# Kernel optimization log

Measured on AMD Instinct MI355X. Metric: run time of the kernel, lower is better.

## Reference

```python
import jax, jax.numpy as jnp
import numpy as np

B, S, D = 16, 2048, 128

def setup_inputs() -> dict:
    key = jax.random.key(0)
    k1, k2, k3 = jax.random.split(key, 3)
    return {
        "query": jax.random.normal(k1, (B, S, D), dtype=jnp.float32),
        "key": jax.random.normal(k2, (B, S, D), dtype=jnp.float32),
        "value": jax.random.normal(k3, (B, S, D), dtype=jnp.float32),
    }

def reference(query, key, value):
    dq = query.shape[-1]
    dk = key.shape[-1]
    # custom scale: sqrt(Dq) + sqrt(Dk - Dq); with Dq == Dk this is sqrt(Dq)
    inv_scale = np.sqrt(dq) + np.sqrt(dk - dq)
    qk = jnp.einsum("bqd,bkd->bqk", query, key) / jnp.float32(inv_scale)
    attn = jax.nn.softmax(qk, axis=-1)  # dropout_p=0 -> identity
    return jnp.einsum("bqk,bkd->bqd", attn, value)
```

## Files before the change

### kernel.cpp

```cpp
#include <hip/hip_runtime.h>
#include <stdint.h>

#define Bn 16
#define Sn 2048
#define Dn 128
#define QBLK 64
#define KVBLK 64
#define NTHR 256
#define NT (Sn / KVBLK)

typedef __attribute__((ext_vector_type(4))) float f32x4;
typedef __attribute__((ext_vector_type(16))) float f32x16;
typedef __attribute__((ext_vector_type(8))) short bf16x8;
typedef __attribute__((ext_vector_type(2))) unsigned int u32x2;

#define SMEM_BYTES 33792

__device__ __forceinline__ uint32_t f2bf_u(float f) {
  return (__float_as_uint(f) + 0x8000u) >> 16;
}
__device__ __forceinline__ uint32_t pk2(float a, float b) {
  return f2bf_u(a) | (f2bf_u(b) << 16);
}

__global__ __launch_bounds__(256) void tr_k(const float* __restrict__ K,
                                            unsigned short* __restrict__ Kf) {
  __shared__ unsigned short lds[64 * 136];
  const int tid = threadIdx.x;
  const float* src = K + (size_t)blockIdx.x * (64 * Dn);
#pragma unroll
  for (int it = 0; it < 8; ++it) {
    const int gr = it * 256 + tid;
    const int k = gr >> 5, g4 = gr & 31;
    const float4 v = ((const float4*)src)[gr];
    unsigned short* p = &lds[k * 136 + g4 * 4];
    p[0] = (unsigned short)f2bf_u(v.x);
    p[1] = (unsigned short)f2bf_u(v.y);
    p[2] = (unsigned short)f2bf_u(v.z);
    p[3] = (unsigned short)f2bf_u(v.w);
  }
  __syncthreads();
  char* dst = (char*)Kf + (size_t)blockIdx.x * 16384;
#pragma unroll
  for (int it = 0; it < 4; ++it) {
    const int g = it * 256 + tid;
    const int lane = g & 63, dk = (g >> 6) & 7, h = g >> 9;
    const int row = 32 * h + (lane & 31);
    const int d0 = dk * 16 + 8 * (lane >> 5);
    const unsigned short* p = &lds[row * 136 + d0];
    uint4 o;
    o.x = (uint32_t)p[0] | ((uint32_t)p[1] << 16);
    o.y = (uint32_t)p[2] | ((uint32_t)p[3] << 16);
    o.z = (uint32_t)p[4] | ((uint32_t)p[5] << 16);
    o.w = (uint32_t)p[6] | ((uint32_t)p[7] << 16);
    *(uint4*)(dst + g * 16) = o;
  }
}

__global__ __launch_bounds__(256) void tr_v(const float* __restrict__ V,
                                            unsigned short* __restrict__ Vf) {
  __shared__ unsigned short lds[64 * 130];
  const int tid = threadIdx.x;
  const float* src = V + (size_t)blockIdx.x * (64 * Dn);
#pragma unroll
  for (int it = 0; it < 8; ++it) {
    const int gr = it * 256 + tid;
    const int k = gr >> 5, g4 = gr & 31;
    const float4 v = ((const float4*)src)[gr];
    unsigned short* p = &lds[k * 130 + g4 * 4];
    p[0] = (unsigned short)f2bf_u(v.x);
    p[1] = (unsigned short)f2bf_u(v.y);
    p[2] = (unsigned short)f2bf_u(v.z);
    p[3] = (unsigned short)f2bf_u(v.w);
  }
  __syncthreads();
  char* dst = (char*)Vf + (size_t)blockIdx.x * 16384;
#pragma unroll
  for (int it = 0; it < 4; ++it) {
    const int g = it * 256 + tid;
    const int lane = g & 63, f3 = (g >> 6) & 7, h = g >> 9;
    const int d = (f3 >> 1) * 32 + (lane & 31);
    const int k0 = 32 * h + (f3 & 1) * 16 + 8 * (lane >> 5);
    uint4 o;
    o.x = (uint32_t)lds[(k0 + 0) * 130 + d] | ((uint32_t)lds[(k0 + 1) * 130 + d] << 16);
    o.y = (uint32_t)lds[(k0 + 2) * 130 + d] | ((uint32_t)lds[(k0 + 3) * 130 + d] << 16);
    o.z = (uint32_t)lds[(k0 + 4) * 130 + d] | ((uint32_t)lds[(k0 + 5) * 130 + d] << 16);
    o.w = (uint32_t)lds[(k0 + 6) * 130 + d] | ((uint32_t)lds[(k0 + 7) * 130 + d] << 16);
    *(uint4*)(dst + g * 16) = o;
  }
}

__global__ __launch_bounds__(NTHR, 2) void attn_fwd(
    const float* __restrict__ Q, const unsigned short* __restrict__ Kf,
    const unsigned short* __restrict__ Vf, float* __restrict__ O) {
  __shared__ uint4 smem_[SMEM_BYTES / 16];
  char* smem = (char*)smem_;

  const int tid = threadIdx.x;
  const int lane = tid & 63;
  const int w = tid >> 6;
  const int qw = w & 1;
  const int h = w >> 1;
  const int hi = lane >> 5;
  const int ql = lane & 31;

  const int i = blockIdx.x;
  const int j = i >> 3;
  const int b = (i & 7) + 8 * (j & 1);
  const int q0 = (j >> 1) * QBLK;
  const int qg = q0 + qw * 32 + ql;

  const float qscale = 0.08838834764831845f * 1.44269504088896340736f;
  bf16x8 qf[8];
  {
    const float* qrow = Q + (size_t)(b * Sn + qg) * Dn;
#pragma unroll
    for (int dk = 0; dk < 8; ++dk) {
      const int d0 = dk * 16 + hi * 8;
      const float4 a = *(const float4*)(qrow + d0);
      const float4 d = *(const float4*)(qrow + d0 + 4);
      bf16x8 q8;
      q8[0] = (short)f2bf_u(a.x * qscale); q8[1] = (short)f2bf_u(a.y * qscale);
      q8[2] = (short)f2bf_u(a.z * qscale); q8[3] = (short)f2bf_u(a.w * qscale);
      q8[4] = (short)f2bf_u(d.x * qscale); q8[5] = (short)f2bf_u(d.y * qscale);
      q8[6] = (short)f2bf_u(d.z * qscale); q8[7] = (short)f2bf_u(d.w * qscale);
      qf[dk] = q8;
    }
  }

  f32x16 o[4];
#pragma unroll
  for (int dt = 0; dt < 4; ++dt) {
#pragma unroll
    for (int jj = 0; jj < 16; ++jj) o[dt][jj] = 0.f;
  }
  float m_r = -1.0e30f, l_r = 0.f;

  const char* Kg = (const char*)(Kf + (size_t)b * Sn * Dn);
  const char* Vg = (const char*)(Vf + (size_t)b * Sn * Dn);

#pragma unroll 2
  for (int t = 0; t < NT; ++t) {
    bf16x8 kfr[8], vfr[8];
    {
      const char* kt = Kg + (size_t)t * 16384 + h * 8192 + lane * 16;
      const char* vt = Vg + (size_t)t * 16384 + h * 8192 + lane * 16;
#pragma unroll
      for (int f = 0; f < 8; ++f) kfr[f] = *(const bf16x8*)(kt + f * 1024);
#pragma unroll
      for (int f = 0; f < 8; ++f) vfr[f] = *(const bf16x8*)(vt + f * 1024);
    }

    f32x16 s;
#pragma unroll
    for (int jj = 0; jj < 16; ++jj) s[jj] = 0.f;
    __builtin_amdgcn_s_setprio(1);
#pragma unroll
    for (int dk = 0; dk < 8; ++dk)
      s = __builtin_amdgcn_mfma_f32_32x32x16_bf16(kfr[dk], qf[dk], s, 0, 0, 0);
    __builtin_amdgcn_s_setprio(0);

    float x0 = fmaxf(fmaxf(s[0], s[1]), fmaxf(s[2], s[3]));
    float x1 = fmaxf(fmaxf(s[4], s[5]), fmaxf(s[6], s[7]));
    float x2 = fmaxf(fmaxf(s[8], s[9]), fmaxf(s[10], s[11]));
    float x3 = fmaxf(fmaxf(s[12], s[13]), fmaxf(s[14], s[15]));
    float pm = fmaxf(fmaxf(x0, x1), fmaxf(x2, x3));
    pm = fmaxf(pm, __shfl_xor(pm, 32, 64));

    if (!__all(pm <= m_r + 8.0f)) {
      const float mnew = fmaxf(m_r, pm);
      const float alpha = __builtin_amdgcn_exp2f(m_r - mnew);
      l_r *= alpha;
#pragma unroll
      for (int dt = 0; dt < 4; ++dt) o[dt] *= alpha;
      m_r = mnew;
    }

#pragma unroll
    for (int jj = 0; jj < 16; ++jj) s[jj] = __builtin_amdgcn_exp2f(s[jj] - m_r);
    {
      float r0 = 0.f, r1 = 0.f, r2 = 0.f, r3 = 0.f;
#pragma unroll
      for (int jj = 0; jj < 4; ++jj) {
        r0 += s[jj]; r1 += s[4 + jj]; r2 += s[8 + jj]; r3 += s[12 + jj];
      }
      float rsum = (r0 + r1) + (r2 + r3);
      l_r += rsum + __shfl_xor(rsum, 32, 64);
    }

    uint32_t own[4][2];
#pragma unroll
    for (int mm = 0; mm < 4; ++mm) {
      own[mm][0] = pk2(s[4 * mm + 0], s[4 * mm + 1]);
      own[mm][1] = pk2(s[4 * mm + 2], s[4 * mm + 3]);
    }
    uint32_t rcv[2][2];
#pragma unroll
    for (int jj = 0; jj < 2; ++jj)
#pragma unroll
      for (int e = 0; e < 2; ++e) {
        uint32_t sel = hi ? own[2 * jj][e] : own[2 * jj + 1][e];
        rcv[jj][e] = (uint32_t)__shfl_xor((int)sel, 32, 64);
      }
    bf16x8 pb[2];
#pragma unroll
    for (int ks = 0; ks < 2; ++ks) {
      union { uint32_t u[4]; bf16x8 v; } tt;
      tt.u[0] = hi ? rcv[ks][0] : own[2 * ks][0];
      tt.u[1] = hi ? rcv[ks][1] : own[2 * ks][1];
      tt.u[2] = hi ? own[2 * ks + 1][0] : rcv[ks][0];
      tt.u[3] = hi ? own[2 * ks + 1][1] : rcv[ks][1];
      pb[ks] = tt.v;
    }

    __builtin_amdgcn_s_setprio(1);
#pragma unroll
    for (int dt = 0; dt < 4; ++dt) {
#pragma unroll
      for (int ks = 0; ks < 2; ++ks) {
        o[dt] = __builtin_amdgcn_mfma_f32_32x32x16_bf16(vfr[dt * 2 + ks], pb[ks],
                                                        o[dt], 0, 0, 0);
      }
    }
    __builtin_amdgcn_s_setprio(0);
  }

  __syncthreads();
  char* xch = smem + qw * 16896;
  if (h) {
#pragma unroll
    for (int dt = 0; dt < 4; ++dt) {
#pragma unroll
      for (int q2 = 0; q2 < 4; ++q2) {
        float4 v;
        v.x = o[dt][4 * q2 + 0]; v.y = o[dt][4 * q2 + 1];
        v.z = o[dt][4 * q2 + 2]; v.w = o[dt][4 * q2 + 3];
        *(float4*)(xch + (dt * 4 + q2) * 1024 + lane * 16) = v;
      }
    }
    *(float2*)(xch + 16384 + lane * 8) = make_float2(m_r, l_r);
  }
  __syncthreads();
  if (!h) {
    const float2 ml1v = *(const float2*)(xch + 16384 + lane * 8);
    const float M = fmaxf(m_r, ml1v.x);
    const float w0 = __builtin_amdgcn_exp2f(m_r - M);
    const float w1 = __builtin_amdgcn_exp2f(ml1v.x - M);
    const float inv = 1.0f / (l_r * w0 + ml1v.y * w1);
    const float s0 = w0 * inv, s1 = w1 * inv;
    float* orow = O + (size_t)(b * Sn + qg) * Dn;
#pragma unroll
    for (int dt = 0; dt < 4; ++dt) {
#pragma unroll
      for (int q2 = 0; q2 < 4; ++q2) {
        const float4 o1v =
            *(const float4*)(xch + (dt * 4 + q2) * 1024 + lane * 16);
        float4 v;
        v.x = o[dt][4 * q2 + 0] * s0 + o1v.x * s1;
        v.y = o[dt][4 * q2 + 1] * s0 + o1v.y * s1;
        v.z = o[dt][4 * q2 + 2] * s0 + o1v.z * s1;
        v.w = o[dt][4 * q2 + 3] * s0 + o1v.w * s1;
        *(float4*)(orow + dt * 32 + q2 * 8 + hi * 4) = v;
      }
    }
  }
}

extern "C" void kernel_launch(void* const* d_in, const int* in_sizes, int n_in,
                              void* d_out, int out_size, void* d_ws, size_t ws_size,
                              hipStream_t stream) {
  (void)in_sizes; (void)n_in; (void)out_size; (void)ws_size;
  const float* Q = (const float*)d_in[0];
  const float* K = (const float*)d_in[1];
  const float* V = (const float*)d_in[2];
  float* O = (float*)d_out;

  unsigned short* Kf = (unsigned short*)d_ws;
  unsigned short* Vf = Kf + (size_t)Bn * Sn * Dn;

  tr_k<<<dim3(Bn * 32, 1, 1), dim3(256, 1, 1), 0, stream>>>(K, Kf);
  tr_v<<<dim3(Bn * 32, 1, 1), dim3(256, 1, 1), 0, stream>>>(V, Vf);
  attn_fwd<<<dim3((Sn / QBLK) * Bn, 1, 1), dim3(NTHR, 1, 1), 0, stream>>>(
      Q, Kf, Vf, O);
}
```

Measured before the change: 68.20 us.

## Double-buffer K/V register fragments and split QK MFMA chain into two accumulators

Replaces the unrolled KV loop with an explicit register double-buffer: the next tile's K/V fragments are loaded before the current tile is computed, with sched_barriers to keep loads ahead of compute. The QK^T product now uses two independent accumulator chains that are summed, which shortens the dependent MFMA chain. The per-tile row-sum shuffle is deferred to a single shuffle after the loop. This costs extra VGPRs for the second fragment set, which may lower occupancy or cause spills.

```diff
diff --git a/kernel.cpp b/kernel.cpp
--- a/kernel.cpp
+++ b/kernel.cpp
@@ -139,92 +139,94 @@
   const char* Kg = (const char*)(Kf + (size_t)b * Sn * Dn);
   const char* Vg = (const char*)(Vf + (size_t)b * Sn * Dn);
 
-#pragma unroll 2
-  for (int t = 0; t < NT; ++t) {
-    bf16x8 kfr[8], vfr[8];
-    {
-      const char* kt = Kg + (size_t)t * 16384 + h * 8192 + lane * 16;
-      const char* vt = Vg + (size_t)t * 16384 + h * 8192 + lane * 16;
-#pragma unroll
-      for (int f = 0; f < 8; ++f) kfr[f] = *(const bf16x8*)(kt + f * 1024);
-#pragma unroll
-      for (int f = 0; f < 8; ++f) vfr[f] = *(const bf16x8*)(vt + f * 1024);
-    }
-
-    f32x16 s;
-#pragma unroll
-    for (int jj = 0; jj < 16; ++jj) s[jj] = 0.f;
-    __builtin_amdgcn_s_setprio(1);
-#pragma unroll
-    for (int dk = 0; dk < 8; ++dk)
-      s = __builtin_amdgcn_mfma_f32_32x32x16_bf16(kfr[dk], qf[dk], s, 0, 0, 0);
-    __builtin_amdgcn_s_setprio(0);
-
-    float x0 = fmaxf(fmaxf(s[0], s[1]), fmaxf(s[2], s[3]));
-    float x1 = fmaxf(fmaxf(s[4], s[5]), fmaxf(s[6], s[7]));
-    float x2 = fmaxf(fmaxf(s[8], s[9]), fmaxf(s[10], s[11]));
-    float x3 = fmaxf(fmaxf(s[12], s[13]), fmaxf(s[14], s[15]));
-    float pm = fmaxf(fmaxf(x0, x1), fmaxf(x2, x3));
-    pm = fmaxf(pm, __shfl_xor(pm, 32, 64));
-
-    if (!__all(pm <= m_r + 8.0f)) {
-      const float mnew = fmaxf(m_r, pm);
-      const float alpha = __builtin_amdgcn_exp2f(m_r - mnew);
-      l_r *= alpha;
-#pragma unroll
-      for (int dt = 0; dt < 4; ++dt) o[dt] *= alpha;
-      m_r = mnew;
-    }
-
-#pragma unroll
-    for (int jj = 0; jj < 16; ++jj) s[jj] = __builtin_amdgcn_exp2f(s[jj] - m_r);
-    {
-      float r0 = 0.f, r1 = 0.f, r2 = 0.f, r3 = 0.f;
-#pragma unroll
-      for (int jj = 0; jj < 4; ++jj) {
-        r0 += s[jj]; r1 += s[4 + jj]; r2 += s[8 + jj]; r3 += s[12 + jj];
-      }
-      float rsum = (r0 + r1) + (r2 + r3);
-      l_r += rsum + __shfl_xor(rsum, 32, 64);
-    }
-
-    uint32_t own[4][2];
-#pragma unroll
-    for (int mm = 0; mm < 4; ++mm) {
-      own[mm][0] = pk2(s[4 * mm + 0], s[4 * mm + 1]);
-      own[mm][1] = pk2(s[4 * mm + 2], s[4 * mm + 3]);
-    }
-    uint32_t rcv[2][2];
-#pragma unroll
-    for (int jj = 0; jj < 2; ++jj)
-#pragma unroll
-      for (int e = 0; e < 2; ++e) {
-        uint32_t sel = hi ? own[2 * jj][e] : own[2 * jj + 1][e];
-        rcv[jj][e] = (uint32_t)__shfl_xor((int)sel, 32, 64);
-      }
-    bf16x8 pb[2];
-#pragma unroll
-    for (int ks = 0; ks < 2; ++ks) {
-      union { uint32_t u[4]; bf16x8 v; } tt;
-      tt.u[0] = hi ? rcv[ks][0] : own[2 * ks][0];
-      tt.u[1] = hi ? rcv[ks][1] : own[2 * ks][1];
-      tt.u[2] = hi ? own[2 * ks + 1][0] : rcv[ks][0];
-      tt.u[3] = hi ? own[2 * ks + 1][1] : rcv[ks][1];
-      pb[ks] = tt.v;
-    }
-
-    __builtin_amdgcn_s_setprio(1);
-#pragma unroll
-    for (int dt = 0; dt < 4; ++dt) {
-#pragma unroll
-      for (int ks = 0; ks < 2; ++ks) {
-        o[dt] = __builtin_amdgcn_mfma_f32_32x32x16_bf16(vfr[dt * 2 + ks], pb[ks],
-                                                        o[dt], 0, 0, 0);
-      }
-    }
-    __builtin_amdgcn_s_setprio(0);
-  }
-
+#define LOADF(kd_, vd_, t_)                                                    \
+  {                                                                            \
+    const char* kt = Kg + (size_t)(t_)*16384 + h * 8192 + lane * 16;           \
+    const char* vt = Vg + (size_t)(t_)*16384 + h * 8192 + lane * 16;           \
+    _Pragma("unroll") for (int f = 0; f < 8; ++f)                              \
+        kd_[f] = *(const bf16x8*)(kt + f * 1024);                              \
+    _Pragma("unroll") for (int f = 0; f < 8; ++f)                              \
+        vd_[f] = *(const bf16x8*)(vt + f * 1024);                              \
+  }
+
+#define TILE(kf_, vf_)                                                         \
+  {                                                                            \
+    f32x16 sa, sb;                                                             \
+    _Pragma("unroll") for (int jj = 0; jj < 16; ++jj) { sa[jj] = 0.f; sb[jj] = 0.f; } \
+    __builtin_amdgcn_s_setprio(1);                                             \
+    _Pragma("unroll") for (int dk = 0; dk < 4; ++dk) {                         \
+      sa = __builtin_amdgcn_mfma_f32_32x32x16_bf16(kf_[dk], qf[dk], sa, 0, 0, 0);       \
+      sb = __builtin_amdgcn_mfma_f32_32x32x16_bf16(kf_[dk + 4], qf[dk + 4], sb, 0, 0, 0);\
+    }                                                                          \
+    __builtin_amdgcn_s_setprio(0);                                             \
+    f32x16 s = sa + sb;                                                        \
+    float x0 = fmaxf(fmaxf(s[0], s[1]), fmaxf(s[2], s[3]));                    \
+    float x1 = fmaxf(fmaxf(s[4], s[5]), fmaxf(s[6], s[7]));                    \
+    float x2 = fmaxf(fmaxf(s[8], s[9]), fmaxf(s[10], s[11]));                  \
+    float x3 = fmaxf(fmaxf(s[12], s[13]), fmaxf(s[14], s[15]));                \
+    float pm = fmaxf(fmaxf(x0, x1), fmaxf(x2, x3));                            \
+    pm = fmaxf(pm, __shfl_xor(pm, 32, 64));                                    \
+    if (!__all(pm <= m_r + 8.0f)) {                                            \
+      const float mnew = fmaxf(m_r, pm);                                       \
+      const float alpha = __builtin_amdgcn_exp2f(m_r - mnew);                  \
+      l_r *= alpha;                                                            \
+      _Pragma("unroll") for (int dt = 0; dt < 4; ++dt) o[dt] *= alpha;         \
+      m_r = mnew;                                                              \
+    }                                                                          \
+    _Pragma("unroll") for (int jj = 0; jj < 16; ++jj)                          \
+        s[jj] = __builtin_amdgcn_exp2f(s[jj] - m_r);                           \
+    {                                                                          \
+      float r0 = 0.f, r1 = 0.f, r2 = 0.f, r3 = 0.f;                            \
+      _Pragma("unroll") for (int jj = 0; jj < 4; ++jj) {                       \
+        r0 += s[jj]; r1 += s[4 + jj]; r2 += s[8 + jj]; r3 += s[12 + jj];       \
+      }                                                                        \
+      l_r += (r0 + r1) + (r2 + r3);      \
+    }                                                                          \
+    uint32_t own[4][2];                                                        \
+    _Pragma("unroll") for (int mm = 0; mm < 4; ++mm) {                         \
+      own[mm][0] = pk2(s[4 * mm + 0], s[4 * mm + 1]);                          \
+      own[mm][1] = pk2(s[4 * mm + 2], s[4 * mm + 3]);                          \
+    }                                                                          \
+    uint32_t rcv[2][2];                                                        \
+    _Pragma("unroll") for (int jj = 0; jj < 2; ++jj)                           \
+        _Pragma("unroll") for (int e = 0; e < 2; ++e) {                        \
+      uint32_t sel = hi ? own[2 * jj][e] : own[2 * jj + 1][e];                 \
+      rcv[jj][e] = (uint32_t)__shfl_xor((int)sel, 32, 64);                     \
+    }                                                                          \
+    bf16x8 pb[2];                                                              \
+    _Pragma("unroll") for (int ks = 0; ks < 2; ++ks) {                         \
+      union { uint32_t u[4]; bf16x8 v; } tt;                                   \
+      tt.u[0] = hi ? rcv[ks][0] : own[2 * ks][0];                              \
+      tt.u[1] = hi ? rcv[ks][1] : own[2 * ks][1];                              \
+      tt.u[2] = hi ? own[2 * ks + 1][0] : rcv[ks][0];                          \
+      tt.u[3] = hi ? own[2 * ks + 1][1] : rcv[ks][1];                          \
+      pb[ks] = tt.v;                                                           \
+    }                                                                          \
+    __builtin_amdgcn_s_setprio(1);                                             \
+    _Pragma("unroll") for (int dt = 0; dt < 4; ++dt) {                         \
+      _Pragma("unroll") for (int ks = 0; ks < 2; ++ks) {                       \
+        o[dt] = __builtin_amdgcn_mfma_f32_32x32x16_bf16(vf_[dt * 2 + ks],      \
+                                                        pb[ks], o[dt], 0, 0, 0);\
+      }                                                                        \
+    }                                                                          \
+    __builtin_amdgcn_s_setprio(0);                                             \
+  }
+
+  bf16x8 kA[8], vA[8], kB[8], vB[8];
+  LOADF(kA, vA, 0)
+  __builtin_amdgcn_sched_barrier(0);
+  for (int t = 0; t < NT; t += 2) {
+    LOADF(kB, vB, t + 1)
+    __builtin_amdgcn_sched_barrier(0);
+    TILE(kA, vA)
+    if (t + 2 < NT) {
+      LOADF(kA, vA, t + 2)
+    }
+    __builtin_amdgcn_sched_barrier(0);
+    TILE(kB, vB)
+  }
+
+  l_r += __shfl_xor(l_r, 32, 64);
   __syncthreads();
   char* xch = smem + qw * 16896;
   if (h) {
```

Result: slower. 97.61 us (+43.1%).

## Split KV sequence across two blocks with combine kernel; fuse K/V conversion

Applied to the files above, without the earlier changes.

Each query tile's key/value range is split into two halves handled by separate blocks, doubling the grid from 512 to 1024 blocks. Each half writes unnormalized partial outputs plus max/sum statistics, and a new combine kernel merges them. The K and V conversion kernels are fused into one launch, the QK MFMA chain is split into two independent accumulators, and the cross-lane row-sum shuffle moves out of the loop. This aims to raise CU occupancy and latency hiding, at the cost of an extra kernel and an extra fp32 output round trip through memory.

```diff
diff --git a/kernel.cpp b/kernel.cpp
--- a/kernel.cpp
+++ b/kernel.cpp
@@ -23,76 +23,82 @@
   return f2bf_u(a) | (f2bf_u(b) << 16);
 }
 
-__global__ __launch_bounds__(256) void tr_k(const float* __restrict__ K,
-                                            unsigned short* __restrict__ Kf) {
+__global__ __launch_bounds__(256) void tr_kv(const float* __restrict__ K,
+                                             const float* __restrict__ V,
+                                             unsigned short* __restrict__ Kf,
+                                             unsigned short* __restrict__ Vf) {
   __shared__ unsigned short lds[64 * 136];
   const int tid = threadIdx.x;
-  const float* src = K + (size_t)blockIdx.x * (64 * Dn);
-#pragma unroll
-  for (int it = 0; it < 8; ++it) {
-    const int gr = it * 256 + tid;
-    const int k = gr >> 5, g4 = gr & 31;
-    const float4 v = ((const float4*)src)[gr];
-    unsigned short* p = &lds[k * 136 + g4 * 4];
-    p[0] = (unsigned short)f2bf_u(v.x);
-    p[1] = (unsigned short)f2bf_u(v.y);
-    p[2] = (unsigned short)f2bf_u(v.z);
-    p[3] = (unsigned short)f2bf_u(v.w);
+  const size_t tileoff = (size_t)blockIdx.x * (64 * Dn);
+
+  {
+    const float* src = K + tileoff;
+#pragma unroll
+    for (int it = 0; it < 8; ++it) {
+      const int gr = it * 256 + tid;
+      const int k = gr >> 5, g4 = gr & 31;
+      const float4 v = ((const float4*)src)[gr];
+      unsigned short* p = &lds[k * 136 + g4 * 4];
+      p[0] = (unsigned short)f2bf_u(v.x);
+      p[1] = (unsigned short)f2bf_u(v.y);
+      p[2] = (unsigned short)f2bf_u(v.z);
+      p[3] = (unsigned short)f2bf_u(v.w);
+    }
+    __syncthreads();
+    char* dst = (char*)Kf + (size_t)blockIdx.x * 16384;
+#pragma unroll
+    for (int it = 0; it < 4; ++it) {
+      const int g = it * 256 + tid;
+      const int lane = g & 63, dk = (g >> 6) & 7, h = g >> 9;
+      const unsigned short* p =
+          &lds[(32 * h + (lane & 31)) * 136 + dk * 16 + 8 * (lane >> 5)];
+      uint4 o;
+      o.x = (uint32_t)p[0] | ((uint32_t)p[1] << 16);
+      o.y = (uint32_t)p[2] | ((uint32_t)p[3] << 16);
+      o.z = (uint32_t)p[4] | ((uint32_t)p[5] << 16);
+      o.w = (uint32_t)p[6] | ((uint32_t)p[7] << 16);
+      *(uint4*)(dst + g * 16) = o;
+    }
   }
   __syncthreads();
-  char* dst = (char*)Kf + (size_t)blockIdx.x * 16384;
-#pragma unroll
-  for (int it = 0; it < 4; ++it) {
-    const int g = it * 256 + tid;
-    const int lane = g & 63, dk = (g >> 6) & 7, h = g >> 9;
-    const int row = 32 * h + (lane & 31);
-    const int d0 = dk * 16 + 8 * (lane >> 5);
-    const unsigned short* p = &lds[row * 136 + d0];
-    uint4 o;
-    o.x = (uint32_t)p[0] | ((uint32_t)p[1] << 16);
-    o.y = (uint32_t)p[2] | ((uint32_t)p[3] << 16);
-    o.z = (uint32_t)p[4] | ((uint32_t)p[5] << 16);
-    o.w = (uint32_t)p[6] | ((uint32_t)p[7] << 16);
-    *(uint4*)(dst + g * 16) = o;
-  }
-}
-
-__global__ __launch_bounds__(256) void tr_v(const float* __restrict__ V,
-                                            unsigned short* __restrict__ Vf) {
-  __shared__ unsigned short lds[64 * 130];
-  const int tid = threadIdx.x;
-  const float* src = V + (size_t)blockIdx.x * (64 * Dn);
-#pragma unroll
-  for (int it = 0; it < 8; ++it) {
-    const int gr = it * 256 + tid;
-    const int k = gr >> 5, g4 = gr & 31;
-    const float4 v = ((const float4*)src)[gr];
-    unsigned short* p = &lds[k * 130 + g4 * 4];
-    p[0] = (unsigned short)f2bf_u(v.x);
-    p[1] = (unsigned short)f2bf_u(v.y);
-    p[2] = (unsigned short)f2bf_u(v.z);
-    p[3] = (unsigned short)f2bf_u(v.w);
-  }
-  __syncthreads();
-  char* dst = (char*)Vf + (size_t)blockIdx.x * 16384;
-#pragma unroll
-  for (int it = 0; it < 4; ++it) {
-    const int g = it * 256 + tid;
-    const int lane = g & 63, f3 = (g >> 6) & 7, h = g >> 9;
-    const int d = (f3 >> 1) * 32 + (lane & 31);
-    const int k0 = 32 * h + (f3 & 1) * 16 + 8 * (lane >> 5);
-    uint4 o;
-    o.x = (uint32_t)lds[(k0 + 0) * 130 + d] | ((uint32_t)lds[(k0 + 1) * 130 + d] << 16);
-    o.y = (uint32_t)lds[(k0 + 2) * 130 + d] | ((uint32_t)lds[(k0 + 3) * 130 + d] << 16);
-    o.z = (uint32_t)lds[(k0 + 4) * 130 + d] | ((uint32_t)lds[(k0 + 5) * 130 + d] << 16);
-    o.w = (uint32_t)lds[(k0 + 6) * 130 + d] | ((uint32_t)lds[(k0 + 7) * 130 + d] << 16);
-    *(uint4*)(dst + g * 16) = o;
-  }
-}
-
+
+  {
+    const float* src = V + tileoff;
+#pragma unroll
+    for (int it = 0; it < 8; ++it) {
+      const int gr = it * 256 + tid;
+      const int k = gr >> 5, g4 = gr & 31;
+      const float4 v = ((const float4*)src)[gr];
+      unsigned short* p = &lds[k * 136 + g4 * 4];
+      p[0] = (unsigned short)f2bf_u(v.x);
+      p[1] = (unsigned short)f2bf_u(v.y);
+      p[2] = (unsigned short)f2bf_u(v.z);
+      p[3] = (unsigned short)f2bf_u(v.w);
+    }
+    __syncthreads();
+    char* dst = (char*)Vf + (size_t)blockIdx.x * 16384;
+#pragma unroll
+    for (int it = 0; it < 4; ++it) {
+      const int g = it * 256 + tid;
+      const int lane = g & 63, f3 = (g >> 6) & 7, h = g >> 9;
+      const int d = (f3 >> 1) * 32 + (lane & 31);
+      const int k0 = 32 * h + (f3 & 1) * 16 + 8 * (lane >> 5);
+      uint4 o;
+      o.x = (uint32_t)lds[(k0 + 0) * 136 + d] | ((uint32_t)lds[(k0 + 1) * 136 + d] << 16);
+      o.y = (uint32_t)lds[(k0 + 2) * 136 + d] | ((uint32_t)lds[(k0 + 3) * 136 + d] << 16);
+      o.z = (uint32_t)lds[(k0 + 4) * 136 + d] | ((uint32_t)lds[(k0 + 5) * 136 + d] << 16);
+      o.w = (uint32_t)lds[(k0 + 6) * 136 + d] | ((uint32_t)lds[(k0 + 7) * 136 + d] << 16);
+      *(uint4*)(dst + g * 16) = o;
+    }
+  }
+}
+
+template <bool SPLIT>
 __global__ __launch_bounds__(NTHR, 2) void attn_fwd(
     const float* __restrict__ Q, const unsigned short* __restrict__ Kf,
-    const unsigned short* __restrict__ Vf, float* __restrict__ O) {
+    const unsigned short* __restrict__ Vf, float* __restrict__ O0,
+    float* __restrict__ O1, float2* __restrict__ ml0,
+    float2* __restrict__ ml1) {
   __shared__ uint4 smem_[SMEM_BYTES / 16];
   char* smem = (char*)smem_;
 
@@ -107,7 +113,11 @@
   const int i = blockIdx.x;
   const int j = i >> 3;
   const int b = (i & 7) + 8 * (j & 1);
-  const int q0 = (j >> 1) * QBLK;
+  const int rest = j >> 1;
+  const int q0 = (rest & 31) * QBLK;
+  const int kvh = SPLIT ? (rest >> 5) : 0;
+  const int nt = SPLIT ? NT / 2 : NT;
+  const int tb = kvh * (NT / 2);
   const int qg = q0 + qw * 32 + ql;
 
   const float qscale = 0.08838834764831845f * 1.44269504088896340736f;
@@ -140,25 +150,28 @@
   const char* Vg = (const char*)(Vf + (size_t)b * Sn * Dn);
 
 #pragma unroll 2
-  for (int t = 0; t < NT; ++t) {
+  for (int t = 0; t < nt; ++t) {
     bf16x8 kfr[8], vfr[8];
     {
-      const char* kt = Kg + (size_t)t * 16384 + h * 8192 + lane * 16;
-      const char* vt = Vg + (size_t)t * 16384 + h * 8192 + lane * 16;
+      const char* kt = Kg + (size_t)(tb + t) * 16384 + h * 8192 + lane * 16;
+      const char* vt = Vg + (size_t)(tb + t) * 16384 + h * 8192 + lane * 16;
 #pragma unroll
       for (int f = 0; f < 8; ++f) kfr[f] = *(const bf16x8*)(kt + f * 1024);
 #pragma unroll
       for (int f = 0; f < 8; ++f) vfr[f] = *(const bf16x8*)(vt + f * 1024);
     }
 
-    f32x16 s;
-#pragma unroll
-    for (int jj = 0; jj < 16; ++jj) s[jj] = 0.f;
+    f32x16 sa, sb;
+#pragma unroll
+    for (int jj = 0; jj < 16; ++jj) { sa[jj] = 0.f; sb[jj] = 0.f; }
     __builtin_amdgcn_s_setprio(1);
 #pragma unroll
-    for (int dk = 0; dk < 8; ++dk)
-      s = __builtin_amdgcn_mfma_f32_32x32x16_bf16(kfr[dk], qf[dk], s, 0, 0, 0);
+    for (int dk = 0; dk < 4; ++dk) {
+      sa = __builtin_amdgcn_mfma_f32_32x32x16_bf16(kfr[dk], qf[dk], sa, 0, 0, 0);
+      sb = __builtin_amdgcn_mfma_f32_32x32x16_bf16(kfr[dk + 4], qf[dk + 4], sb, 0, 0, 0);
+    }
     __builtin_amdgcn_s_setprio(0);
+    f32x16 s = sa + sb;
 
     float x0 = fmaxf(fmaxf(s[0], s[1]), fmaxf(s[2], s[3]));
     float x1 = fmaxf(fmaxf(s[4], s[5]), fmaxf(s[6], s[7]));
@@ -184,8 +197,7 @@
       for (int jj = 0; jj < 4; ++jj) {
         r0 += s[jj]; r1 += s[4 + jj]; r2 += s[8 + jj]; r3 += s[12 + jj];
       }
-      float rsum = (r0 + r1) + (r2 + r3);
-      l_r += rsum + __shfl_xor(rsum, 32, 64);
+      l_r += (r0 + r1) + (r2 + r3);
     }
 
     uint32_t own[4][2];
@@ -225,6 +237,7 @@
     __builtin_amdgcn_s_setprio(0);
   }
 
+  l_r += __shfl_xor(l_r, 32, 64);
   __syncthreads();
   char* xch = smem + qw * 16896;
   if (h) {
@@ -246,40 +259,93 @@
     const float M = fmaxf(m_r, ml1v.x);
     const float w0 = __builtin_amdgcn_exp2f(m_r - M);
     const float w1 = __builtin_amdgcn_exp2f(ml1v.x - M);
-    const float inv = 1.0f / (l_r * w0 + ml1v.y * w1);
-    const float s0 = w0 * inv, s1 = w1 * inv;
-    float* orow = O + (size_t)(b * Sn + qg) * Dn;
-#pragma unroll
-    for (int dt = 0; dt < 4; ++dt) {
-#pragma unroll
-      for (int q2 = 0; q2 < 4; ++q2) {
-        const float4 o1v =
-            *(const float4*)(xch + (dt * 4 + q2) * 1024 + lane * 16);
-        float4 v;
-        v.x = o[dt][4 * q2 + 0] * s0 + o1v.x * s1;
-        v.y = o[dt][4 * q2 + 1] * s0 + o1v.y * s1;
-        v.z = o[dt][4 * q2 + 2] * s0 + o1v.z * s1;
-        v.w = o[dt][4 * q2 + 3] * s0 + o1v.w * s1;
-        *(float4*)(orow + dt * 32 + q2 * 8 + hi * 4) = v;
-      }
-    }
-  }
+    const float lsum = l_r * w0 + ml1v.y * w1;
+    if (SPLIT) {
+      float* Op = kvh ? O1 : O0;
+      float2* ml = kvh ? ml1 : ml0;
+      const int rowb = b * Sn + qg;
+      float* orow = Op + (size_t)rowb * Dn;
+#pragma unroll
+      for (int dt = 0; dt < 4; ++dt) {
+#pragma unroll
+        for (int q2 = 0; q2 < 4; ++q2) {
+          const float4 o1v =
+              *(const float4*)(xch + (dt * 4 + q2) * 1024 + lane * 16);
+          float4 v;
+          v.x = o[dt][4 * q2 + 0] * w0 + o1v.x * w1;
+          v.y = o[dt][4 * q2 + 1] * w0 + o1v.y * w1;
+          v.z = o[dt][4 * q2 + 2] * w0 + o1v.z * w1;
+          v.w = o[dt][4 * q2 + 3] * w0 + o1v.w * w1;
+          *(float4*)(orow + dt * 32 + q2 * 8 + hi * 4) = v;
+        }
+      }
+      ml[rowb] = make_float2(M, lsum);
+    } else {
+      const float inv = 1.0f / lsum;
+      const float s0 = w0 * inv, s1 = w1 * inv;
+      float* orow = O0 + (size_t)(b * Sn + qg) * Dn;
+#pragma unroll
+      for (int dt = 0; dt < 4; ++dt) {
+#pragma unroll
+        for (int q2 = 0; q2 < 4; ++q2) {
+          const float4 o1v =
+              *(const float4*)(xch + (dt * 4 + q2) * 1024 + lane * 16);
+          float4 v;
+          v.x = o[dt][4 * q2 + 0] * s0 + o1v.x * s1;
+          v.y = o[dt][4 * q2 + 1] * s0 + o1v.y * s1;
+          v.z = o[dt][4 * q2 + 2] * s0 + o1v.z * s1;
+          v.w = o[dt][4 * q2 + 3] * s0 + o1v.w * s1;
+          *(float4*)(orow + dt * 32 + q2 * 8 + hi * 4) = v;
+        }
+      }
+    }
+  }
+}
+
+__global__ __launch_bounds__(256) void attn_combine(
+    float* __restrict__ O, const float* __restrict__ O1,
+    const float2* __restrict__ ml0, const float2* __restrict__ ml1) {
+  const int e = blockIdx.x * 256 + threadIdx.x;
+  const int row = e >> 5;
+  const float2 a = ml0[row];
+  const float2 bb = ml1[row];
+  const float M = fmaxf(a.x, bb.x);
+  const float w0 = __builtin_amdgcn_exp2f(a.x - M);
+  const float w1 = __builtin_amdgcn_exp2f(bb.x - M);
+  const float inv = 1.0f / (w0 * a.y + w1 * bb.y);
+  const float s0 = w0 * inv, s1 = w1 * inv;
+  f32x4 o0 = ((const f32x4*)O)[e];
+  f32x4 o1 = ((const f32x4*)O1)[e];
+  ((f32x4*)O)[e] = o0 * s0 + o1 * s1;
 }
 
 extern "C" void kernel_launch(void* const* d_in, const int* in_sizes, int n_in,
                               void* d_out, int out_size, void* d_ws, size_t ws_size,
                               hipStream_t stream) {
-  (void)in_sizes; (void)n_in; (void)out_size; (void)ws_size;
+  (void)in_sizes; (void)n_in; (void)out_size;
   const float* Q = (const float*)d_in[0];
   const float* K = (const float*)d_in[1];
   const float* V = (const float*)d_in[2];
   float* O = (float*)d_out;
 
+  const size_t nE = (size_t)Bn * Sn * Dn;
   unsigned short* Kf = (unsigned short*)d_ws;
-  unsigned short* Vf = Kf + (size_t)Bn * Sn * Dn;
-
-  tr_k<<<dim3(Bn * 32, 1, 1), dim3(256, 1, 1), 0, stream>>>(K, Kf);
-  tr_v<<<dim3(Bn * 32, 1, 1), dim3(256, 1, 1), 0, stream>>>(V, Vf);
-  attn_fwd<<<dim3((Sn / QBLK) * Bn, 1, 1), dim3(NTHR, 1, 1), 0, stream>>>(
-      Q, Kf, Vf, O);
-}
+  unsigned short* Vf = Kf + nE;
+  const size_t baseB = nE * 2 * 2;
+  const size_t needSplit = baseB + nE * 4 + (size_t)Bn * Sn * 8 * 2;
+
+  tr_kv<<<dim3(Bn * 32, 1, 1), dim3(256, 1, 1), 0, stream>>>(K, V, Kf, Vf);
+
+  if (ws_size >= needSplit) {
+    float* O1 = (float*)((char*)d_ws + baseB);
+    float2* ml0 = (float2*)((char*)d_ws + baseB + nE * 4);
+    float2* ml1 = ml0 + (size_t)Bn * Sn;
+    attn_fwd<true><<<dim3((Sn / QBLK) * Bn * 2, 1, 1), dim3(NTHR, 1, 1), 0,
+                     stream>>>(Q, Kf, Vf, O, O1, ml0, ml1);
+    attn_combine<<<dim3((int)(nE / 4 / 256), 1, 1), dim3(256, 1, 1), 0,
+                   stream>>>(O, O1, ml0, ml1);
+  } else {
+    attn_fwd<false><<<dim3((Sn / QBLK) * Bn, 1, 1), dim3(NTHR, 1, 1), 0,
+                      stream>>>(Q, Kf, Vf, O, nullptr, nullptr, nullptr);
+  }
+}
```

Result: slower. 76.82 us (+12.6%).
